# Optimization experiments

Hardware: AMD Instinct MI355X
Metric: run time of the kernel (lower is better)

The kernel has to match this reference:

```python
import jax, jax.numpy as jnp
import numpy as np


def setup_inputs() -> dict:
    key = jax.random.key(0)
    k1, k2 = jax.random.split(key)
    B, C, H, W = 4, 128, 192, 640
    left = jax.random.normal(k1, (B, C, H, W), dtype=jnp.float32)
    right = jax.random.normal(k2, (B, C, H, W), dtype=jnp.float32)
    return {"left": left, "right": right, "num_disparities": 96}


def reference(left, right, num_disparities):
    """Dot-product stereo cost volume (is_right=False).

    cost[b, d, y, x] = sum_c left[b, c, y, x] * right[b, c, y, x - d],
    with zeros where x - d < 0.  Output: [B, D, H, W].
    """
    D = num_disparities
    B, C, H, W = left.shape
    # Zero-pad right on the left edge of the width axis so that the slice
    # starting at (D-1-d) gives right shifted by d with zero fill.
    right_pad = jnp.pad(right, ((0, 0), (0, 0), (0, 0), (D - 1, 0)))

    def per_disparity(d):
        r = jax.lax.dynamic_slice_in_dim(right_pad, (D - 1) - d, W, axis=3)
        return jnp.sum(left * r, axis=1)  # [B, H, W], reduce over channels

    cost = jax.lax.map(per_disparity, jnp.arange(D))  # [D, B, H, W]
    return jnp.transpose(cost, (1, 0, 2, 3))  # [B, D, H, W]
```

## Files before the change

### kernel.cpp

```cpp
#include <hip/hip_runtime.h>

#define Bn 4
#define Cn 128
#define Hn 192
#define Wn 640
#define Dn 96

#define CK 32
#define XB 128
#define UB 224
#define FP 228
#define RP 40
#define EP 132

typedef float f32x4 __attribute__((ext_vector_type(4)));
typedef short short8 __attribute__((ext_vector_type(8)));

__device__ __forceinline__ unsigned short f2bf(float f) {
  unsigned int u = __builtin_bit_cast(unsigned int, f);
  u += 0x7FFFu + ((u >> 16) & 1u);
  return (unsigned short)(u >> 16);
}

struct SStage {
  unsigned short Fb[CK * FP];
  unsigned short Rb[UB * RP];
  unsigned short Lb[XB * RP];
};
union SMem {
  SStage s;
  float epi[Dn * EP];
};

__global__ __launch_bounds__(256, 3) void cost_volume_kernel(
    const float* __restrict__ left, const float* __restrict__ right,
    float* __restrict__ out) {
  __shared__ SMem sm;

  const int x0 = blockIdx.x * XB;
  const int y  = blockIdx.y;
  const int b  = blockIdx.z;
  const int t  = threadIdx.x;
  const int w  = t >> 6;
  const int l  = t & 63;
  const int n  = l & 15;
  const int q  = l >> 4;

  f32x4 acc[2][7];
#pragma unroll
  for (int i = 0; i < 2; ++i)
#pragma unroll
    for (int j = 0; j < 7; ++j) acc[i][j] = (f32x4){0.f, 0.f, 0.f, 0.f};

  const int tc = t >> 3;
  const int tv = t & 7;
  const size_t rowbase = ((size_t)b * Cn * Hn + (size_t)y) * Wn;
  const float* lrow0 = left + rowbase + x0;
  const float* rrow0 = right + rowbase + (x0 - 96);

  for (int ck = 0; ck < Cn; ck += CK) {
    const size_t coff = (size_t)(ck + tc) * (Hn * Wn);

    {
      const float* rp = rrow0 + coff;
#pragma unroll
      for (int i = 0; i < 7; ++i) {
        const int uv = tv + (i << 3);
        const int ue = uv << 2;
        f32x4 v = (f32x4){0.f, 0.f, 0.f, 0.f};
        if (x0 - 96 + ue >= 0) v = *(const f32x4*)(rp + ue);
        ushort4 h;
        h.x = f2bf(v.x); h.y = f2bf(v.y); h.z = f2bf(v.z); h.w = f2bf(v.w);
        *(ushort4*)&sm.s.Fb[tc * FP + ue] = h;
      }
    }
    __syncthreads();

    {
#pragma unroll
      for (int i = 0; i < 8; ++i) {
        const int cq = (t & 1) + ((i & 3) << 1);
        const int u  = ((i >> 2) << 7) + (t >> 1);
        if (u < UB) {
          const int c4 = cq << 2;
          ushort4 h;
          h.x = sm.s.Fb[(c4 + 0) * FP + u];
          h.y = sm.s.Fb[(c4 + 1) * FP + u];
          h.z = sm.s.Fb[(c4 + 2) * FP + u];
          h.w = sm.s.Fb[(c4 + 3) * FP + u];
          *(ushort4*)&sm.s.Rb[u * RP + c4] = h;
        }
      }
    }
    __syncthreads();

    {
      const float* lp = lrow0 + coff;
#pragma unroll
      for (int i = 0; i < 4; ++i) {
        const int uv = tv + (i << 3);
        const int ue = uv << 2;
        f32x4 v = *(const f32x4*)(lp + ue);
        ushort4 h;
        h.x = f2bf(v.x); h.y = f2bf(v.y); h.z = f2bf(v.z); h.w = f2bf(v.w);
        *(ushort4*)&sm.s.Fb[tc * FP + ue] = h;
      }
    }
    __syncthreads();

    {
#pragma unroll
      for (int i = 0; i < 4; ++i) {
        const int cq = (t & 1) + (i << 1);
        const int u  = t >> 1;
        const int c4 = cq << 2;
        ushort4 h;
        h.x = sm.s.Fb[(c4 + 0) * FP + u];
        h.y = sm.s.Fb[(c4 + 1) * FP + u];
        h.z = sm.s.Fb[(c4 + 2) * FP + u];
        h.w = sm.s.Fb[(c4 + 3) * FP + u];
        *(ushort4*)&sm.s.Lb[u * RP + c4] = h;
      }
    }
    __syncthreads();

    {
      const short8 b0 = *(const short8*)&sm.s.Lb[(32 * w + n) * RP + q * 8];
      const short8 b1 = *(const short8*)&sm.s.Lb[(32 * w + 16 + n) * RP + q * 8];
#pragma unroll
      for (int j = 0; j < 8; ++j) {
        const short8 a = *(const short8*)&sm.s.Rb[(32 * w + 16 * j + n) * RP + q * 8];
        if (j < 7)
          acc[0][j] = __builtin_amdgcn_mfma_f32_16x16x32_bf16(a, b0, acc[0][j], 0, 0, 0);
        if (j > 0)
          acc[1][j - 1] = __builtin_amdgcn_mfma_f32_16x16x32_bf16(a, b1, acc[1][j - 1], 0, 0, 0);
      }
    }
    __syncthreads();
  }

#pragma unroll
  for (int i = 0; i < 2; ++i) {
    const int xl = 32 * w + 16 * i + n;
#pragma unroll
    for (int j = 0; j < 7; ++j) {
      const int jj = j + i;
#pragma unroll
      for (int r = 0; r < 4; ++r) {
        const int d = (16 * i + n) - (16 * jj + 4 * q + r) + 96;
        if (d >= 0 && d < Dn) sm.epi[d * EP + xl] = acc[i][j][r];
      }
    }
  }
  __syncthreads();

  {
    const size_t obase = ((size_t)b * Dn * Hn + (size_t)y) * Wn + x0;
    const int xv = (t & 31) << 2;
    const int d0 = t >> 5;
#pragma unroll
    for (int ii = 0; ii < 12; ++ii) {
      const int d = d0 + (ii << 3);
      f32x4 v = *(const f32x4*)&sm.epi[d * EP + xv];
      *(f32x4*)&out[obase + (size_t)d * (Hn * Wn) + xv] = v;
    }
  }
}

extern "C" void kernel_launch(void* const* d_in, const int* in_sizes, int n_in,
                              void* d_out, int out_size, void* d_ws, size_t ws_size,
                              hipStream_t stream) {
  const float* left  = (const float*)d_in[0];
  const float* right = (const float*)d_in[1];
  float* out = (float*)d_out;
  dim3 grid(Wn / XB, Hn, Bn);
  cost_volume_kernel<<<grid, dim3(256, 1, 1), 0, stream>>>(left, right, out);
}
```

Before: 568.2 us.

## Halve x-tile, drop LDS transpose, prefetch next channel chunk into registers

The x-tile shrinks from 128 to 64 columns, so each wave now owns 16 pixels and 7 MFMA tiles. The separate LDS transpose passes are removed: the MFMA operands are gathered as strided 16-bit LDS reads from a channel-major, swizzled layout. The next 32-channel chunk is loaded from global memory and converted to bf16 in registers while the current chunk is being computed, which cuts the number of barriers per chunk. LDS per block drops, occupancy rises to 6 blocks per SIMD, and the epilogue runs in two 48-disparity halves. In exchange, right-image data is re-read more often across neighbouring tiles, and the scalar LDS gathers cost more instructions.

```diff
diff --git a/kernel.cpp b/kernel.cpp
--- a/kernel.cpp
+++ b/kernel.cpp
@@ -5,13 +5,11 @@
 #define Hn 192
 #define Wn 640
 #define Dn 96
+#define HW (Hn * Wn)
 
-#define CK 32
-#define XB 128
-#define UB 224
-#define FP 228
-#define RP 40
-#define EP 132
+#define PR 184
+#define PL 88
+#define EP 68
 
 typedef float f32x4 __attribute__((ext_vector_type(4)));
 typedef short short8 __attribute__((ext_vector_type(8)));
@@ -22,147 +20,108 @@
   return (unsigned short)(u >> 16);
 }
 
-struct SStage {
-  unsigned short Fb[CK * FP];
-  unsigned short Rb[UB * RP];
-  unsigned short Lb[XB * RP];
-};
 union SMem {
-  SStage s;
-  float epi[Dn * EP];
+  struct {
+    unsigned short R[32 * PR];
+    unsigned short L[32 * PL];
+  } s;
+  float epi[48 * EP];
 };
 
-__global__ __launch_bounds__(256, 3) void cost_volume_kernel(
+__global__ __launch_bounds__(256, 6) void cost_volume_kernel(
     const float* __restrict__ left, const float* __restrict__ right,
     float* __restrict__ out) {
   __shared__ SMem sm;
 
-  const int x0 = blockIdx.x * XB;
+  const int x0 = blockIdx.x * 64;
   const int y  = blockIdx.y;
   const int b  = blockIdx.z;
   const int t  = threadIdx.x;
   const int w  = t >> 6;
-  const int l  = t & 63;
-  const int n  = l & 15;
-  const int q  = l >> 4;
+  const int n  = t & 15;
+  const int q  = (t >> 4) & 3;
 
-  f32x4 acc[2][7];
+  f32x4 acc[7];
 #pragma unroll
-  for (int i = 0; i < 2; ++i)
+  for (int jj = 0; jj < 7; ++jj) acc[jj] = (f32x4){0.f, 0.f, 0.f, 0.f};
+
+  const int tc  = t >> 3;
+  const int tv  = t & 7;
+  const int swz = (tc >> 3) & 3;
+  const float* lrow = left  + ((size_t)(b * Cn) * Hn + y) * Wn + x0;
+  const float* rrow = right + ((size_t)(b * Cn) * Hn + y) * Wn + x0 - 96;
+
+  ushort4 hv[7];
+  auto load_chunk = [&](int ck) {
+    const size_t coff = (size_t)(ck + tc) * HW;
 #pragma unroll
-    for (int j = 0; j < 7; ++j) acc[i][j] = (f32x4){0.f, 0.f, 0.f, 0.f};
+    for (int i = 0; i < 5; ++i) {
+      const int ue = 4 * tv + 32 * i;
+      f32x4 v = (f32x4){0.f, 0.f, 0.f, 0.f};
+      if (x0 + ue >= 96) v = *(const f32x4*)(rrow + coff + ue);
+      hv[i].x = f2bf(v.x); hv[i].y = f2bf(v.y); hv[i].z = f2bf(v.z); hv[i].w = f2bf(v.w);
+    }
+#pragma unroll
+    for (int i = 0; i < 2; ++i) {
+      const int ue = 4 * tv + 32 * i;
+      f32x4 v = *(const f32x4*)(lrow + coff + ue);
+      hv[5 + i].x = f2bf(v.x); hv[5 + i].y = f2bf(v.y);
+      hv[5 + i].z = f2bf(v.z); hv[5 + i].w = f2bf(v.w);
+    }
+  };
 
-  const int tc = t >> 3;
-  const int tv = t & 7;
-  const size_t rowbase = ((size_t)b * Cn * Hn + (size_t)y) * Wn;
-  const float* lrow0 = left + rowbase + x0;
-  const float* rrow0 = right + rowbase + (x0 - 96);
-
-  for (int ck = 0; ck < Cn; ck += CK) {
-    const size_t coff = (size_t)(ck + tc) * (Hn * Wn);
+  load_chunk(0);
+#pragma unroll
+  for (int kk = 0; kk < 4; ++kk) {
+    __syncthreads();
+#pragma unroll
+    for (int i = 0; i < 5; ++i) {
+      const int ue = 4 * tv + 32 * i;
+      *(ushort4*)&sm.s.R[tc * PR + ue + 8 * swz] = hv[i];
+    }
+#pragma unroll
+    for (int i = 0; i < 2; ++i) {
+      const int ue = 4 * tv + 32 * i;
+      *(ushort4*)&sm.s.L[tc * PL + ue + 8 * swz] = hv[5 + i];
+    }
+    __syncthreads();
+    if (kk < 3) load_chunk(32 * (kk + 1));
 
     {
-      const float* rp = rrow0 + coff;
+      const unsigned short* Lp = &sm.s.L[(8 * q) * PL + 16 * w + n + 8 * q];
+      short8 bf;
 #pragma unroll
-      for (int i = 0; i < 7; ++i) {
-        const int uv = tv + (i << 3);
-        const int ue = uv << 2;
-        f32x4 v = (f32x4){0.f, 0.f, 0.f, 0.f};
-        if (x0 - 96 + ue >= 0) v = *(const f32x4*)(rp + ue);
-        ushort4 h;
-        h.x = f2bf(v.x); h.y = f2bf(v.y); h.z = f2bf(v.z); h.w = f2bf(v.w);
-        *(ushort4*)&sm.s.Fb[tc * FP + ue] = h;
+      for (int j = 0; j < 8; ++j) bf[j] = (short)Lp[j * PL];
+      const unsigned short* Rp = &sm.s.R[(8 * q) * PR + 16 * w + n + 8 * q];
+#pragma unroll
+      for (int jj = 0; jj < 7; ++jj) {
+        short8 af;
+#pragma unroll
+        for (int j = 0; j < 8; ++j) af[j] = (short)Rp[j * PR + 16 * jj];
+        acc[jj] = __builtin_amdgcn_mfma_f32_16x16x32_bf16(af, bf, acc[jj], 0, 0, 0);
       }
     }
-    __syncthreads();
-
-    {
-#pragma unroll
-      for (int i = 0; i < 8; ++i) {
-        const int cq = (t & 1) + ((i & 3) << 1);
-        const int u  = ((i >> 2) << 7) + (t >> 1);
-        if (u < UB) {
-          const int c4 = cq << 2;
-          ushort4 h;
-          h.x = sm.s.Fb[(c4 + 0) * FP + u];
-          h.y = sm.s.Fb[(c4 + 1) * FP + u];
-          h.z = sm.s.Fb[(c4 + 2) * FP + u];
-          h.w = sm.s.Fb[(c4 + 3) * FP + u];
-          *(ushort4*)&sm.s.Rb[u * RP + c4] = h;
-        }
-      }
-    }
-    __syncthreads();
-
-    {
-      const float* lp = lrow0 + coff;
-#pragma unroll
-      for (int i = 0; i < 4; ++i) {
-        const int uv = tv + (i << 3);
-        const int ue = uv << 2;
-        f32x4 v = *(const f32x4*)(lp + ue);
-        ushort4 h;
-        h.x = f2bf(v.x); h.y = f2bf(v.y); h.z = f2bf(v.z); h.w = f2bf(v.w);
-        *(ushort4*)&sm.s.Fb[tc * FP + ue] = h;
-      }
-    }
-    __syncthreads();
-
-    {
-#pragma unroll
-      for (int i = 0; i < 4; ++i) {
-        const int cq = (t & 1) + (i << 1);
-        const int u  = t >> 1;
-        const int c4 = cq << 2;
-        ushort4 h;
-        h.x = sm.s.Fb[(c4 + 0) * FP + u];
-        h.y = sm.s.Fb[(c4 + 1) * FP + u];
-        h.z = sm.s.Fb[(c4 + 2) * FP + u];
-        h.w = sm.s.Fb[(c4 + 3) * FP + u];
-        *(ushort4*)&sm.s.Lb[u * RP + c4] = h;
-      }
-    }
-    __syncthreads();
-
-    {
-      const short8 b0 = *(const short8*)&sm.s.Lb[(32 * w + n) * RP + q * 8];
-      const short8 b1 = *(const short8*)&sm.s.Lb[(32 * w + 16 + n) * RP + q * 8];
-#pragma unroll
-      for (int j = 0; j < 8; ++j) {
-        const short8 a = *(const short8*)&sm.s.Rb[(32 * w + 16 * j + n) * RP + q * 8];
-        if (j < 7)
-          acc[0][j] = __builtin_amdgcn_mfma_f32_16x16x32_bf16(a, b0, acc[0][j], 0, 0, 0);
-        if (j > 0)
-          acc[1][j - 1] = __builtin_amdgcn_mfma_f32_16x16x32_bf16(a, b1, acc[1][j - 1], 0, 0, 0);
-      }
-    }
-    __syncthreads();
   }
 
 #pragma unroll
-  for (int i = 0; i < 2; ++i) {
-    const int xl = 32 * w + 16 * i + n;
+  for (int p = 0; p < 2; ++p) {
+    __syncthreads();
 #pragma unroll
-    for (int j = 0; j < 7; ++j) {
-      const int jj = j + i;
+    for (int jj = 0; jj < 7; ++jj)
 #pragma unroll
       for (int r = 0; r < 4; ++r) {
-        const int d = (16 * i + n) - (16 * jj + 4 * q + r) + 96;
-        if (d >= 0 && d < Dn) sm.epi[d * EP + xl] = acc[i][j][r];
+        const int d = 96 + n - 16 * jj - 4 * q - r - 48 * p;
+        if (d >= 0 && d < 48) sm.epi[d * EP + 16 * w + n] = acc[jj][r];
       }
-    }
-  }
-  __syncthreads();
-
-  {
-    const size_t obase = ((size_t)b * Dn * Hn + (size_t)y) * Wn + x0;
-    const int xv = (t & 31) << 2;
-    const int d0 = t >> 5;
+    __syncthreads();
+    const size_t obase = (((size_t)b * Dn + 48 * p) * Hn + y) * Wn + x0;
+    const int tx = (t & 15) << 2;
+    const int d0 = t >> 4;
 #pragma unroll
-    for (int ii = 0; ii < 12; ++ii) {
-      const int d = d0 + (ii << 3);
-      f32x4 v = *(const f32x4*)&sm.epi[d * EP + xv];
-      *(f32x4*)&out[obase + (size_t)d * (Hn * Wn) + xv] = v;
+    for (int ii = 0; ii < 3; ++ii) {
+      const int d = d0 + 16 * ii;
+      f32x4 v = *(const f32x4*)&sm.epi[d * EP + tx];
+      *(f32x4*)&out[obase + (size_t)d * HW + tx] = v;
     }
   }
 }
@@ -173,6 +132,6 @@
   const float* left  = (const float*)d_in[0];
   const float* right = (const float*)d_in[1];
   float* out = (float*)d_out;
-  dim3 grid(Wn / XB, Hn, Bn);
+  dim3 grid(Wn / 64, Hn, Bn);
   cost_volume_kernel<<<grid, dim3(256, 1, 1), 0, stream>>>(left, right, out);
 }
```

New measurement: 553.5 us. 2.6% less time.
